# Kernel tuning notes

Measured on AMD Instinct MI355X. Metric: run time of the kernel, lower is better.

The kernel has to match this reference:

```python
import jax, jax.numpy as jnp
import numpy as np

NEG = -1e9

def gat_layer(x, edge_mask, W, al, ar, rW, b, act):
    # x: (B, N, Fin); edge_mask: (B, N, N) bool, edge u->v at [b,u,v]
    B, N, _ = x.shape
    H, D = al.shape
    f = (x @ W).reshape(B, N, H, D)                      # (B,N,H,D)
    el = jnp.einsum('bnhd,hd->bnh', f, al)               # src term
    er = jnp.einsum('bnhd,hd->bnh', f, ar)               # dst term
    # e[b,u,v,h] = LeakyReLU(el[src=u] + er[dst=v]), slope 0.2 (dgl default)
    e = jax.nn.leaky_relu(el[:, :, None, :] + er[:, None, :, :], 0.2)
    logits = jnp.where(edge_mask[..., None], e, NEG)
    # masked, empty-column-safe softmax over incoming edges (axis=1 = src u)
    m = jnp.max(logits, axis=1, keepdims=True)
    p = jnp.exp(logits - m) * edge_mask[..., None]
    alpha = p / jnp.clip(jnp.sum(p, axis=1, keepdims=True), 1e-9)
    out = jnp.einsum('buvh,buhd->bvhd', alpha, f)        # scatter-sum to dst
    res = (x @ rW).reshape(B, N, H, D)                   # residual projection
    out = out + res + b.reshape(H, D)
    return act(out) if act is not None else out


def setup_inputs() -> dict:
    key = jax.random.key(0)
    ks = jax.random.split(key, 12)
    n, c, h, w = 16, 64, 32, 32
    num_s, hid, H = 64, 64, 4
    seg = jax.random.normal(ks[0], (n, c, h, w), dtype=jnp.float32)
    adj = jax.random.normal(ks[1], (n, h * w, h * w), dtype=jnp.float32)
    s = 0.1
    return {
        'seg': seg, 'adj': adj,
        'W0': jax.random.normal(ks[2], (num_s, H * hid), dtype=jnp.float32) * s,
        'al0': jax.random.normal(ks[3], (H, hid), dtype=jnp.float32) * s,
        'ar0': jax.random.normal(ks[4], (H, hid), dtype=jnp.float32) * s,
        'rW0': jax.random.normal(ks[5], (num_s, H * hid), dtype=jnp.float32) * s,
        'b0': jnp.zeros((H * hid,), dtype=jnp.float32),
        'W1': jax.random.normal(ks[6], (H * hid, H * num_s), dtype=jnp.float32) * s,
        'al1': jax.random.normal(ks[7], (H, num_s), dtype=jnp.float32) * s,
        'ar1': jax.random.normal(ks[8], (H, num_s), dtype=jnp.float32) * s,
        'rW1': jax.random.normal(ks[9], (H * hid, H * num_s), dtype=jnp.float32) * s,
        'b1': jnp.zeros((H * num_s,), dtype=jnp.float32),
    }


def reference(seg, adj, W0, al0, ar0, rW0, b0, W1, al1, ar1, rW1, b1):
    n, c, h, w = seg.shape
    num_s = W0.shape[0]
    x = seg.reshape(n, -1, num_s)                        # (n, N, num_s)
    k = (h * w) // 6
    topv, _ = jax.lax.top_k(adj, k)
    thr = topv[..., -1]                                  # k-th largest per row
    adj_t = jnp.where(adj >= thr[..., None], adj, 0.0)
    edge_mask = adj_t > 0                                # (n, N, N)
    fea = gat_layer(x, edge_mask, W0, al0, ar0, rW0, b0, jax.nn.elu)
    fea = fea.reshape(n, fea.shape[1], -1)               # flatten heads
    fea = gat_layer(fea, edge_mask, W1, al1, ar1, rW1, b1, None)
    out = fea.mean(axis=2)                               # mean over heads -> (n, N, num_s)
    return out.reshape(n, -1, num_s)
```

## Files before the change

### kernel.cpp

```cpp
#include <hip/hip_runtime.h>
#include <hip/hip_bf16.h>
#include <stdint.h>

#define BB   16
#define NN   1024
#define KSEL 170
#define LOG2E 1.4426950408889634f
#define HP   264

typedef __attribute__((ext_vector_type(8))) short short8;
typedef __attribute__((ext_vector_type(4))) short short4v;
typedef __attribute__((ext_vector_type(4))) float f32x4;
typedef __attribute__((ext_vector_type(2))) float float2v;

static __device__ __forceinline__ short f2bf(float x) {
    __hip_bfloat16 h = __float2bfloat16(x);
    return *reinterpret_cast<short*>(&h);
}
static __device__ __forceinline__ float bf2f(short x) {
    uint32_t u = ((uint32_t)(uint16_t)x) << 16;
    return __uint_as_float(u);
}
static __device__ __forceinline__ float fast_exp2(float x) {
    float r; asm("v_exp_f32 %0, %1" : "=v"(r) : "v"(x)); return r;
}

__global__ __launch_bounds__(256) void k_topk_mask(
    const float* __restrict__ adj, uint64_t* __restrict__ mask,
    const float* __restrict__ W0, const float* __restrict__ rW0,
    const float* __restrict__ W1, const float* __restrict__ rW1,
    const float* __restrict__ seg,
    short* __restrict__ Wt0, short* __restrict__ rWt0,
    short* __restrict__ Wt1, short* __restrict__ rWt1,
    short* __restrict__ xb0)
{
    const int bid = blockIdx.x, t = threadIdx.x;
    if (bid >= 4096) {
        const int pid = bid - 4096;
        if (pid < 64) {
            int idx = pid * 256 + t;
            int o = idx >> 6, k = idx & 63;
            Wt0[idx] = f2bf(W0[(size_t)k * 256 + o]);
        } else if (pid < 128) {
            int idx = (pid - 64) * 256 + t;
            int o = idx >> 6, k = idx & 63;
            rWt0[idx] = f2bf(rW0[(size_t)k * 256 + o]);
        } else if (pid < 384) {
            int idx = (pid - 128) * 256 + t;
            int o = idx >> 8, k = idx & 255;
            Wt1[idx] = f2bf(W1[(size_t)k * 256 + o]);
        } else if (pid < 640) {
            int idx = (pid - 384) * 256 + t;
            int o = idx >> 8, k = idx & 255;
            rWt1[idx] = f2bf(rW1[(size_t)k * 256 + o]);
        } else {
            int i = ((pid - 640) * 256 + t) * 4;
            float4 v = *(const float4*)(seg + i);
            short4v o4;
            o4[0] = f2bf(v.x); o4[1] = f2bf(v.y); o4[2] = f2bf(v.z); o4[3] = f2bf(v.w);
            *(short4v*)(xb0 + i) = o4;
        }
        return;
    }

    const int wid = t >> 6, lane = t & 63;
    const int row = bid * 4 + wid;
    const float* a = adj + (size_t)row * NN;
    __shared__ uint32_t hist[4][4 * HP];
    uint32_t* h = &hist[wid][0];
    uint32_t* hs = &hist[wid][(lane >> 4) * HP];

    uint32_t key[16];
    #pragma unroll
    for (int j = 0; j < 16; ++j) {
        uint32_t u = __float_as_uint(a[lane + j * 64]);
        key[j] = u ^ ((u >> 31) ? 0xFFFFFFFFu : 0x80000000u);
    }

    uint32_t prefix = 0u, kk = KSEL;
    #pragma unroll
    for (int pass = 0; pass < 2; ++pass) {
        const int shift = 24 - 8 * pass;
        const uint32_t hi_mask = pass ? 0xFF000000u : 0u;
        #pragma unroll
        for (int s4 = 0; s4 < 4; ++s4)
            *(uint4*)&h[s4 * HP + lane * 4] = make_uint4(0u, 0u, 0u, 0u);
        __builtin_amdgcn_wave_barrier();
        #pragma unroll
        for (int j = 0; j < 16; ++j)
            if ((key[j] & hi_mask) == prefix)
                atomicAdd(&hs[(key[j] >> shift) & 255], 1u);
        __builtin_amdgcn_wave_barrier();
        uint4 c0 = *(const uint4*)&h[lane * 4];
        uint4 c1 = *(const uint4*)&h[HP + lane * 4];
        uint4 c2 = *(const uint4*)&h[2 * HP + lane * 4];
        uint4 c3 = *(const uint4*)&h[3 * HP + lane * 4];
        uint4 c4;
        c4.x = c0.x + c1.x + c2.x + c3.x;
        c4.y = c0.y + c1.y + c2.y + c3.y;
        c4.z = c0.z + c1.z + c2.z + c3.z;
        c4.w = c0.w + c1.w + c2.w + c3.w;
        const uint32_t T = c4.x + c4.y + c4.z + c4.w;
        uint32_t s = T;
        #pragma unroll
        for (int off = 1; off < 64; off <<= 1) {
            uint32_t v = __shfl_down(s, off);
            s += (lane + off < 64) ? v : 0u;
        }
        const uint32_t E = s - T;
        const uint32_t s3 = c4.w;
        const uint32_t s2 = c4.z + s3;
        const uint32_t s1 = c4.y + s2;
        const uint32_t s0 = c4.x + s1;
        const uint32_t ci[4] = {c4.x, c4.y, c4.z, c4.w};
        const uint32_t si[4] = {s0, s1, s2, s3};
        uint32_t found = 0u, nb = 0u, nk = 0u;
        #pragma unroll
        for (int i = 0; i < 4; ++i) {
            uint32_t incl = E + si[i];
            uint32_t excl = incl - ci[i];
            if (excl < kk && kk <= incl) { found = 1u; nb = (uint32_t)(lane * 4 + i); nk = kk - excl; }
        }
        uint64_t bal = __ballot(found != 0u);
        int wl = __ffsll((unsigned long long)bal) - 1;
        prefix = prefix | ((uint32_t)__shfl((int)nb, wl) << shift);
        kk = (uint32_t)__shfl((int)nk, wl);
    }

    uint32_t sv[16];
    #pragma unroll
    for (int j = 0; j < 16; ++j)
        sv[j] = ((key[j] ^ prefix) >> 16) == 0u ? key[j] : 0u;

    uint32_t thr_key;
    for (;;) {
        uint32_t m = 0u;
        #pragma unroll
        for (int j = 0; j < 16; ++j) m = m > sv[j] ? m : sv[j];
        #pragma unroll
        for (int off = 1; off < 64; off <<= 1) {
            uint32_t v = __shfl_xor(m, off);
            m = m > v ? m : v;
        }
        if (m == 0u) { thr_key = 0u; break; }
        uint32_t c = 0u;
        #pragma unroll
        for (int j = 0; j < 16; ++j) c += (sv[j] == m) ? 1u : 0u;
        #pragma unroll
        for (int off = 1; off < 64; off <<= 1)
            c += __shfl_xor(c, off);
        if (kk <= c) { thr_key = m; break; }
        kk -= c;
        #pragma unroll
        for (int j = 0; j < 16; ++j) if (sv[j] == m) sv[j] = 0u;
    }

    #pragma unroll
    for (int j = 0; j < 16; ++j) {
        bool pred = (key[j] >= thr_key) && (key[j] > 0x80000000u);
        uint64_t bal = __ballot(pred);
        if (lane == 0) mask[(size_t)row * 16 + j] = bal;
    }
}

template<int K>
__global__ __launch_bounds__(256, 2) void k_features_mfma(
    const short* __restrict__ xb,
    const short* __restrict__ Wt,
    const short* __restrict__ rWt,
    const float* __restrict__ al,
    const float* __restrict__ ar,
    short* __restrict__ ft,
    short* __restrict__ fea,
    float* __restrict__ el_t,
    float* __restrict__ er_t,
    const uint64_t* __restrict__ mask, uint64_t* __restrict__ maskT, int nfeat)
{
    const int bid = blockIdx.x;
    const int tid = threadIdx.x;
    if (bid >= nfeat) {
        const int tile = (bid - nfeat) * 4 + (tid >> 6);
        const int lane = tid & 63;
        const int b  = tile >> 8;
        const int uw = (tile >> 4) & 15;
        const int vw = tile & 15;
        const size_t bN = (size_t)b * NN;
        uint64_t w = mask[(bN + uw * 64 + lane) * 16 + vw];
        uint64_t r_out = 0;
        #pragma unroll
        for (int j = 0; j < 64; ++j) {
            uint64_t r = __ballot((w >> j) & 1ull);
            if (lane == j) r_out = r;
        }
        maskT[(bN + vw * 64 + lane) * 16 + uw] = r_out;
        return;
    }

    const int lane = tid & 63, hh = tid >> 6;
    const int l15 = lane & 15, l4 = lane >> 4;
    const int n0 = bid * 32;
    const int b_idx = n0 >> 10;
    const int nloc = n0 & (NN - 1);
    const int bh = b_idx * 4 + hh;
    const int XP = K + 8;

    __shared__ short x_lds[32 * (K + 8)];

    const int CH = K / 8;
    #pragma unroll
    for (int c = tid; c < 32 * CH; c += 256) {
        const int row = c / CH, col = c - row * CH;
        *(short8*)&x_lds[row * XP + col * 8] =
            *(const short8*)(xb + ((size_t)n0 + row) * K + col * 8);
    }
    __syncthreads();

    const short* wbase = Wt  + (size_t)(hh * 64 + l15) * K + l4 * 8;
    const short* rbase = rWt + (size_t)(hh * 64 + l15) * K + l4 * 8;
    const size_t qs = (size_t)16 * K;

    f32x4 accf[2][4], accr[2][4];
    #pragma unroll
    for (int s = 0; s < 2; ++s)
        #pragma unroll
        for (int q = 0; q < 4; ++q) {
            accf[s][q] = (f32x4){0.f, 0.f, 0.f, 0.f};
            accr[s][q] = (f32x4){0.f, 0.f, 0.f, 0.f};
        }

    short8 bufW[2][4], bufR[2][4];
    #pragma unroll
    for (int q = 0; q < 4; ++q) {
        bufW[0][q] = *(const short8*)(wbase + q * qs);
        bufR[0][q] = *(const short8*)(rbase + q * qs);
    }

    #pragma unroll
    for (int ks = 0; ks < K / 32; ++ks) {
        const int cur = ks & 1, nxt = cur ^ 1;
        if (ks + 1 < K / 32) {
            #pragma unroll
            for (int q = 0; q < 4; ++q) {
                bufW[nxt][q] = *(const short8*)(wbase + q * qs + (ks + 1) * 32);
                bufR[nxt][q] = *(const short8*)(rbase + q * qs + (ks + 1) * 32);
            }
            __builtin_amdgcn_sched_barrier(0);
        }
        short8 x0 = *(const short8*)&x_lds[l15 * XP + ks * 32 + l4 * 8];
        short8 x1 = *(const short8*)&x_lds[(16 + l15) * XP + ks * 32 + l4 * 8];
        #pragma unroll
        for (int q = 0; q < 4; ++q) {
            accf[0][q] = __builtin_amdgcn_mfma_f32_16x16x32_bf16(x0, bufW[cur][q], accf[0][q], 0, 0, 0);
            accf[1][q] = __builtin_amdgcn_mfma_f32_16x16x32_bf16(x1, bufW[cur][q], accf[1][q], 0, 0, 0);
            accr[0][q] = __builtin_amdgcn_mfma_f32_16x16x32_bf16(bufR[cur][q], x0, accr[0][q], 0, 0, 0);
            accr[1][q] = __builtin_amdgcn_mfma_f32_16x16x32_bf16(bufR[cur][q], x1, accr[1][q], 0, 0, 0);
        }
    }

    #pragma unroll
    for (int s = 0; s < 2; ++s) {
        const int nl = nloc + s * 16;
        #pragma unroll
        for (int q = 0; q < 4; ++q) {
            short4v pk;
            #pragma unroll
            for (int r = 0; r < 4; ++r) pk[r] = f2bf(accf[s][q][r]);
            const int dl = q * 16 + l15;
            const size_t idx = ((size_t)bh << 16)
                             + (size_t)(nl >> 6) * 4096
                             + (size_t)(((nl & 63) >> 3) + (l4 >> 1)) * 512
                             + (size_t)dl * 8 + (l4 & 1) * 4;
            *(short4v*)(ft + idx) = pk;
        }
        float elv[4] = {0.f, 0.f, 0.f, 0.f}, erv[4] = {0.f, 0.f, 0.f, 0.f};
        #pragma unroll
        for (int q = 0; q < 4; ++q) {
            const float alv = al[hh * 64 + q * 16 + l15];
            const float arv = ar[hh * 64 + q * 16 + l15];
            #pragma unroll
            for (int r = 0; r < 4; ++r) {
                elv[r] = fmaf(accf[s][q][r], alv, elv[r]);
                erv[r] = fmaf(accf[s][q][r], arv, erv[r]);
            }
        }
        #pragma unroll
        for (int r = 0; r < 4; ++r) {
            #pragma unroll
            for (int off = 1; off < 16; off <<= 1) {
                elv[r] += __shfl_xor(elv[r], off);
                erv[r] += __shfl_xor(erv[r], off);
            }
        }
        if (l15 == 0) {
            float4 e4, r4;
            e4.x = elv[0] * LOG2E; e4.y = elv[1] * LOG2E;
            e4.z = elv[2] * LOG2E; e4.w = elv[3] * LOG2E;
            r4.x = erv[0] * LOG2E; r4.y = erv[1] * LOG2E;
            r4.z = erv[2] * LOG2E; r4.w = erv[3] * LOG2E;
            *(float4*)(el_t + (size_t)bh * NN + nl + l4 * 4) = e4;
            *(float4*)(er_t + (size_t)bh * NN + nl + l4 * 4) = r4;
        }
        #pragma unroll
        for (int q = 0; q < 4; ++q) {
            short4v pk;
            #pragma unroll
            for (int r = 0; r < 4; ++r) pk[r] = f2bf(accr[s][q][r]);
            *(short4v*)(fea + ((size_t)n0 + s * 16 + l15) * 256 + hh * 64 + q * 16 + l4 * 4) = pk;
        }
    }
}

template<int ELU_ON>
__global__ __launch_bounds__(256, 4) void k_attn(
    const short* __restrict__ ft,
    const float* __restrict__ el_t,
    const float* __restrict__ er_t,
    const uint64_t* __restrict__ maskT,
    const float* __restrict__ bias,
    short* fea)
{
    const int id = blockIdx.x;
    const int swz = (id & 7) * 128 + (id >> 3);
    const int b  = swz >> 6;
    const int h  = (swz >> 4) & 3;
    const int vt = swz & 15;
    const int tid = threadIdx.x;
    const int lane = tid & 63, wid = tid >> 6;
    const int l15 = lane & 15, l4 = lane >> 4;
    const int bh = b * 4 + h;
    const size_t bN = (size_t)b * NN;
    const int v0 = vt * 64;

    __shared__ __align__(16) short f_lds[3][4096];
    __shared__ __align__(16) float el_lds[NN];
    __shared__ __align__(16) uint64_t m_lds[64 * 17];
    __shared__ float smax[4];

    const short* gsrc = ft + ((size_t)bh << 16);

    {
        short8 sa = *(const short8*)(gsrc + tid * 8);
        short8 sb = *(const short8*)(gsrc + 2048 + tid * 8);
        float4 ev4 = ((const float4*)(el_t + (size_t)bh * NN))[tid];
        ((float4*)el_lds)[tid] = ev4;
        float m = fmaxf(fmaxf(ev4.x, ev4.y), fmaxf(ev4.z, ev4.w));
        #pragma unroll
        for (int off = 32; off; off >>= 1) m = fmaxf(m, __shfl_xor(m, off));
        if (lane == 0) smax[wid] = m;
        #pragma unroll
        for (int i = 0; i < 4; ++i) {
            int idx = tid + i * 256;
            m_lds[(idx >> 4) * 17 + (idx & 15)] =
                maskT[(bN + v0 + (idx >> 4)) * 16 + (idx & 15)];
        }
        *(short8*)&f_lds[0][tid * 8] = sa;
        *(short8*)&f_lds[0][2048 + tid * 8] = sb;
    }

    short8 Aa = *(const short8*)(gsrc + 4096 + tid * 8);
    short8 Ab = *(const short8*)(gsrc + 4096 + 2048 + tid * 8);

    const int vlo = wid * 16 + l15;
    const float er_lo = er_t[(size_t)bh * NN + v0 + vlo];

    __syncthreads();

    const float emx = fmaxf(fmaxf(smax[0], smax[1]), fmaxf(smax[2], smax[3]));
    const float e0 = emx + er_lo;
    const float cv_lo = fmaxf(e0, 0.2f * e0);
    const float c1_lo = er_lo - cv_lo, c2_lo = 0.2f * er_lo - cv_lo;
    const float2v c1s = {c1_lo, c1_lo};
    const float2v c2s = {c2_lo, c2_lo};
    const float2v k02 = {0.2f, 0.2f};

    const uint8_t* mbytes = (const uint8_t*)m_lds;
    const int moff_lo = vlo * 136;

    short8 ones8;
    #pragma unroll
    for (int i = 0; i < 8; ++i) ones8[i] = (short)0x3F80;

    f32x4 accLo[4];
    #pragma unroll
    for (int i = 0; i < 4; ++i) accLo[i] = (f32x4){0.f, 0.f, 0.f, 0.f};
    f32x4 dLo = (f32x4){0.f, 0.f, 0.f, 0.f};

    auto compute = [&](const short* fb, int tt) {
        #pragma unroll
        for (int kc = 0; kc < 2; ++kc) {
            const float2v* ep2 = (const float2v*)&el_lds[tt * 64 + kc * 32 + l4 * 8];
            uint32_t mLo = mbytes[moff_lo + tt * 8 + kc * 4 + l4];
            short8 aLo;
            #pragma unroll
            for (int jj = 0; jj < 4; ++jj) {
                float2v e2 = ep2[jj];
                float2v arg = __builtin_elementwise_max(e2 + c1s, e2 * k02 + c2s);
                float p0 = ((mLo >> (2 * jj)) & 1u)     ? fast_exp2(arg.x) : 0.f;
                float p1 = ((mLo >> (2 * jj + 1)) & 1u) ? fast_exp2(arg.y) : 0.f;
                aLo[2 * jj]     = f2bf(p0);
                aLo[2 * jj + 1] = f2bf(p1);
            }
            const int fo = (kc * 4 + l4) * 512 + l15 * 8;
            short8 bw0 = *(const short8*)(fb + fo);
            short8 bw1 = *(const short8*)(fb + fo + 128);
            short8 bw2 = *(const short8*)(fb + fo + 256);
            short8 bw3 = *(const short8*)(fb + fo + 384);
            __builtin_amdgcn_s_setprio(1);
            accLo[0] = __builtin_amdgcn_mfma_f32_16x16x32_bf16(aLo, bw0, accLo[0], 0, 0, 0);
            accLo[1] = __builtin_amdgcn_mfma_f32_16x16x32_bf16(aLo, bw1, accLo[1], 0, 0, 0);
            accLo[2] = __builtin_amdgcn_mfma_f32_16x16x32_bf16(aLo, bw2, accLo[2], 0, 0, 0);
            accLo[3] = __builtin_amdgcn_mfma_f32_16x16x32_bf16(aLo, bw3, accLo[3], 0, 0, 0);
            dLo      = __builtin_amdgcn_mfma_f32_16x16x32_bf16(aLo, ones8, dLo, 0, 0, 0);
            __builtin_amdgcn_s_setprio(0);
        }
    };

    short8 Ba, Bb;
    #pragma unroll 1
    for (int tt = 0; tt < 16; tt += 2) {
        if (tt + 2 < 16) {
            Ba = *(const short8*)(gsrc + (tt + 2) * 4096 + tid * 8);
            Bb = *(const short8*)(gsrc + (tt + 2) * 4096 + 2048 + tid * 8);
            __builtin_amdgcn_sched_barrier(0);
        }
        compute(f_lds[tt % 3], tt);
        {
            short* dst = f_lds[(tt + 1) % 3];
            *(short8*)&dst[tid * 8] = Aa;
            *(short8*)&dst[2048 + tid * 8] = Ab;
        }
        __syncthreads();
        if (tt + 3 < 16) {
            Aa = *(const short8*)(gsrc + (tt + 3) * 4096 + tid * 8);
            Ab = *(const short8*)(gsrc + (tt + 3) * 4096 + 2048 + tid * 8);
            __builtin_amdgcn_sched_barrier(0);
        }
        compute(f_lds[(tt + 1) % 3], tt + 1);
        if (tt + 2 < 16) {
            short* dst = f_lds[(tt + 2) % 3];
            *(short8*)&dst[tid * 8] = Ba;
            *(short8*)&dst[2048 + tid * 8] = Bb;
            __syncthreads();
        }
    }

    float rcpLo[4];
    #pragma unroll
    for (int r = 0; r < 4; ++r)
        rcpLo[r] = 1.f / fmaxf(dLo[r], 1e-9f);
    #pragma unroll
    for (int dt = 0; dt < 4; ++dt) {
        const int d = dt * 16 + l15;
        const float bv = bias[h * 64 + d];
        #pragma unroll
        for (int r = 0; r < 4; ++r) {
            const int vl = v0 + wid * 16 + l4 * 4 + r;
            const size_t rowL = (bN + vl) * 256 + h * 64 + d;
            float ov = accLo[dt][r] * rcpLo[r] + bf2f(fea[rowL]) + bv;
            if (ELU_ON) ov = ov > 0.f ? ov : __expf(ov) - 1.f;
            fea[rowL] = f2bf(ov);
        }
    }
}

__global__ __launch_bounds__(256) void k_headmean(
    const short* __restrict__ fea, float* __restrict__ outp)
{
    const int i = (blockIdx.x * 256 + threadIdx.x) * 8;
    const int d0 = i & 63;
    const size_t node = (size_t)(i >> 6);
    const short* p = fea + node * 256 + d0;
    short8 h0 = *(const short8*)(p);
    short8 h1 = *(const short8*)(p + 64);
    short8 h2 = *(const short8*)(p + 128);
    short8 h3 = *(const short8*)(p + 192);
    float4 o0, o1;
    #pragma unroll
    for (int j = 0; j < 4; ++j) {
        float v = 0.25f * (bf2f(h0[j]) + bf2f(h1[j]) + bf2f(h2[j]) + bf2f(h3[j]));
        (&o0.x)[j] = v;
    }
    #pragma unroll
    for (int j = 0; j < 4; ++j) {
        float v = 0.25f * (bf2f(h0[4 + j]) + bf2f(h1[4 + j]) + bf2f(h2[4 + j]) + bf2f(h3[4 + j]));
        (&o1.x)[j] = v;
    }
    *(float4*)(outp + i) = o0;
    *(float4*)(outp + i + 4) = o1;
}

extern "C" void kernel_launch(void* const* d_in, const int* in_sizes, int n_in,
                              void* d_out, int out_size, void* d_ws, size_t ws_size,
                              hipStream_t stream) {
    const float* seg = (const float*)d_in[0];
    const float* adj = (const float*)d_in[1];
    const float* W0  = (const float*)d_in[2];
    const float* al0 = (const float*)d_in[3];
    const float* ar0 = (const float*)d_in[4];
    const float* rW0 = (const float*)d_in[5];
    const float* b0  = (const float*)d_in[6];
    const float* W1  = (const float*)d_in[7];
    const float* al1 = (const float*)d_in[8];
    const float* ar1 = (const float*)d_in[9];
    const float* rW1 = (const float*)d_in[10];
    const float* b1  = (const float*)d_in[11];
    float* out = (float*)d_out;

    char* ws = (char*)d_ws;
    size_t off = 0;
    uint64_t* mask  = (uint64_t*)ws;
    off += (size_t)BB * NN * 16 * 8;
    uint64_t* maskT = (uint64_t*)(ws + off); off += (size_t)BB * NN * 16 * 8;
    short* ftb = (short*)(ws + off); off += (size_t)BB * 256 * NN * 2;
    short* fea = (short*)(ws + off); off += (size_t)BB * NN * 256 * 2;
    short* xb0 = (short*)(ws + off); off += (size_t)BB * NN * 64 * 2;
    short* Wt0  = (short*)(ws + off); off += 256 * 64 * 2;
    short* rWt0 = (short*)(ws + off); off += 256 * 64 * 2;
    short* Wt1  = (short*)(ws + off); off += 256 * 256 * 2;
    short* rWt1 = (short*)(ws + off); off += 256 * 256 * 2;
    float* el   = (float*)(ws + off); off += (size_t)BB * 4 * NN * 4;
    float* er   = (float*)(ws + off); off += (size_t)BB * 4 * NN * 4;

    k_topk_mask<<<4096 + 1664, 256, 0, stream>>>(adj, mask, W0, rW0, W1, rW1, seg,
                                                 Wt0, rWt0, Wt1, rWt1, xb0);

    k_features_mfma<64><<<512 + 1024, 256, 0, stream>>>(xb0, Wt0, rWt0, al0, ar0,
                                                        ftb, fea, el, er,
                                                        mask, maskT, 512);
    k_attn<1><<<1024, 256, 0, stream>>>(ftb, el, er, maskT, b0, fea);
    k_features_mfma<256><<<512, 256, 0, stream>>>(fea, Wt1, rWt1, al1, ar1,
                                                  ftb, fea, el, er,
                                                  mask, maskT, 512);
    k_attn<0><<<1024, 256, 0, stream>>>(ftb, el, er, maskT, b1, fea);

    k_headmean<<<BB * NN * 64 / 2048, 256, 0, stream>>>(fea, out);
}
```

Baseline: 140.5 us.

## Preload mask bits into registers and double-buffer two source tiles per stage

The per-row edge-mask bytes are now read straight from global memory into packed registers at kernel start, replacing the shared-memory mask staging buffer and its byte loads in the inner loop. The three-slot single-tile LDS ring becomes a two-slot buffer holding two 64-row source tiles per stage, and the loop is fully unrolled into eight stages, which halves the number of block barriers. The cost is more registers held live (four short8 prefetch regs plus eight mask words), which may lower occupancy. LDS use stays roughly the same.

```diff
diff --git a/kernel.cpp b/kernel.cpp
--- a/kernel.cpp
+++ b/kernel.cpp
@@ -331,36 +331,44 @@
     const size_t bN = (size_t)b * NN;
     const int v0 = vt * 64;
 
-    __shared__ __align__(16) short f_lds[3][4096];
+    __shared__ __align__(16) short f_lds[2][8192];
     __shared__ __align__(16) float el_lds[NN];
-    __shared__ __align__(16) uint64_t m_lds[64 * 17];
     __shared__ float smax[4];
 
     const short* gsrc = ft + ((size_t)bh << 16);
-
+    const int vlo = wid * 16 + l15;
+
+    uint32_t pkm[8];
     {
-        short8 sa = *(const short8*)(gsrc + tid * 8);
-        short8 sb = *(const short8*)(gsrc + 2048 + tid * 8);
+        const uint4* mr = (const uint4*)(maskT + (size_t)(bN + v0 + vlo) * 16);
+        #pragma unroll
+        for (int i = 0; i < 8; ++i) {
+            uint4 q = mr[i];
+            uint32_t b0a = (q.x >> (8 * l4)) & 0xFFu;
+            uint32_t b1a = (q.y >> (8 * l4)) & 0xFFu;
+            uint32_t b0b = (q.z >> (8 * l4)) & 0xFFu;
+            uint32_t b1b = (q.w >> (8 * l4)) & 0xFFu;
+            pkm[i] = b0a | (b1a << 8) | (b0b << 16) | (b1b << 24);
+        }
+    }
+
+    {
+        short8 s0 = *(const short8*)(gsrc + tid * 8);
+        short8 s1 = *(const short8*)(gsrc + 2048 + tid * 8);
+        short8 s2 = *(const short8*)(gsrc + 4096 + tid * 8);
+        short8 s3 = *(const short8*)(gsrc + 6144 + tid * 8);
         float4 ev4 = ((const float4*)(el_t + (size_t)bh * NN))[tid];
         ((float4*)el_lds)[tid] = ev4;
         float m = fmaxf(fmaxf(ev4.x, ev4.y), fmaxf(ev4.z, ev4.w));
         #pragma unroll
         for (int off = 32; off; off >>= 1) m = fmaxf(m, __shfl_xor(m, off));
         if (lane == 0) smax[wid] = m;
-        #pragma unroll
-        for (int i = 0; i < 4; ++i) {
-            int idx = tid + i * 256;
-            m_lds[(idx >> 4) * 17 + (idx & 15)] =
-                maskT[(bN + v0 + (idx >> 4)) * 16 + (idx & 15)];
-        }
-        *(short8*)&f_lds[0][tid * 8] = sa;
-        *(short8*)&f_lds[0][2048 + tid * 8] = sb;
-    }
-
-    short8 Aa = *(const short8*)(gsrc + 4096 + tid * 8);
-    short8 Ab = *(const short8*)(gsrc + 4096 + 2048 + tid * 8);
-
-    const int vlo = wid * 16 + l15;
+        *(short8*)&f_lds[0][tid * 8] = s0;
+        *(short8*)&f_lds[0][2048 + tid * 8] = s1;
+        *(short8*)&f_lds[0][4096 + tid * 8] = s2;
+        *(short8*)&f_lds[0][6144 + tid * 8] = s3;
+    }
+
     const float er_lo = er_t[(size_t)bh * NN + v0 + vlo];
 
     __syncthreads();
@@ -373,9 +381,6 @@
     const float2v c2s = {c2_lo, c2_lo};
     const float2v k02 = {0.2f, 0.2f};
 
-    const uint8_t* mbytes = (const uint8_t*)m_lds;
-    const int moff_lo = vlo * 136;
-
     short8 ones8;
     #pragma unroll
     for (int i = 0; i < 8; ++i) ones8[i] = (short)0x3F80;
@@ -385,11 +390,11 @@
     for (int i = 0; i < 4; ++i) accLo[i] = (f32x4){0.f, 0.f, 0.f, 0.f};
     f32x4 dLo = (f32x4){0.f, 0.f, 0.f, 0.f};
 
-    auto compute = [&](const short* fb, int tt) {
+    auto computeHalf = [&](const short* fb, int tt, uint32_t m0, uint32_t m1) {
         #pragma unroll
         for (int kc = 0; kc < 2; ++kc) {
             const float2v* ep2 = (const float2v*)&el_lds[tt * 64 + kc * 32 + l4 * 8];
-            uint32_t mLo = mbytes[moff_lo + tt * 8 + kc * 4 + l4];
+            uint32_t mLo = kc ? m1 : m0;
             short8 aLo;
             #pragma unroll
             for (int jj = 0; jj < 4; ++jj) {
@@ -415,31 +420,26 @@
         }
     };
 
-    short8 Ba, Bb;
-    #pragma unroll 1
-    for (int tt = 0; tt < 16; tt += 2) {
-        if (tt + 2 < 16) {
-            Ba = *(const short8*)(gsrc + (tt + 2) * 4096 + tid * 8);
-            Bb = *(const short8*)(gsrc + (tt + 2) * 4096 + 2048 + tid * 8);
+    short8 Ra, Rb, Rc, Rd;
+    #pragma unroll
+    for (int i = 0; i < 8; ++i) {
+        if (i < 7) {
+            const short* ps = gsrc + (size_t)(2 * i + 2) * 4096;
+            Ra = *(const short8*)(ps + tid * 8);
+            Rb = *(const short8*)(ps + 2048 + tid * 8);
+            Rc = *(const short8*)(ps + 4096 + tid * 8);
+            Rd = *(const short8*)(ps + 6144 + tid * 8);
             __builtin_amdgcn_sched_barrier(0);
         }
-        compute(f_lds[tt % 3], tt);
-        {
-            short* dst = f_lds[(tt + 1) % 3];
-            *(short8*)&dst[tid * 8] = Aa;
-            *(short8*)&dst[2048 + tid * 8] = Ab;
-        }
-        __syncthreads();
-        if (tt + 3 < 16) {
-            Aa = *(const short8*)(gsrc + (tt + 3) * 4096 + tid * 8);
-            Ab = *(const short8*)(gsrc + (tt + 3) * 4096 + 2048 + tid * 8);
-            __builtin_amdgcn_sched_barrier(0);
-        }
-        compute(f_lds[(tt + 1) % 3], tt + 1);
-        if (tt + 2 < 16) {
-            short* dst = f_lds[(tt + 2) % 3];
-            *(short8*)&dst[tid * 8] = Ba;
-            *(short8*)&dst[2048 + tid * 8] = Bb;
+        const short* fb = f_lds[i & 1];
+        computeHalf(fb,        2 * i,     (pkm[i] >> 0) & 0xFFu,  (pkm[i] >> 8) & 0xFFu);
+        computeHalf(fb + 4096, 2 * i + 1, (pkm[i] >> 16) & 0xFFu, (pkm[i] >> 24) & 0xFFu);
+        if (i < 7) {
+            short* dst = f_lds[(i + 1) & 1];
+            *(short8*)&dst[tid * 8] = Ra;
+            *(short8*)&dst[2048 + tid * 8] = Rb;
+            *(short8*)&dst[4096 + tid * 8] = Rc;
+            *(short8*)&dst[6144 + tid * 8] = Rd;
             __syncthreads();
         }
     }
```

Measured after the change: 143.3 us. Within noise of the previous version (+2.0%).
